# Optimization experiments

Hardware: AMD Instinct MI355X
Metric: run time of the kernel (lower is better)

## Reference

```python
import jax, jax.numpy as jnp
import numpy as np

B, S, D, H, E, K = 2, 2048, 512, 2048, 16, 2
LN_EPS = 1e-5


def setup_inputs() -> dict:
    key = jax.random.key(0)
    ks = jax.random.split(key, 9)
    s_in = 1.0 / np.sqrt(D)
    s_hid = 1.0 / np.sqrt(H)
    return {
        "x": jax.random.normal(ks[0], (B, S, D), dtype=jnp.float32),
        "Wg": jax.random.normal(ks[1], (D, E), dtype=jnp.float32) * s_in,
        "bg": jax.random.normal(ks[2], (E,), dtype=jnp.float32) * 0.01,
        "W1": jax.random.normal(ks[3], (E, D, H), dtype=jnp.float32) * s_in,
        "b1": jax.random.normal(ks[4], (E, H), dtype=jnp.float32) * 0.01,
        "W2": jax.random.normal(ks[5], (E, H, D), dtype=jnp.float32) * s_hid,
        "b2": jax.random.normal(ks[6], (E, D), dtype=jnp.float32) * 0.01,
        "gamma": jnp.ones((D,), dtype=jnp.float32),
        "beta": jnp.zeros((D,), dtype=jnp.float32),
    }


def reference(x, Wg, bg, W1, b1, W2, b2, gamma, beta):
    # --- top-k gating (GatingFuncTopK) ---
    logits = jnp.einsum("bsd,de->bse", x, Wg) + bg            # [B,S,E]
    probs = jax.nn.softmax(logits, axis=-1)
    topk_vals, topk_idx = jax.lax.top_k(probs, K)             # [B,S,K]
    # scatter top-k probs back into a sparse [B,S,E] routing matrix
    sparse = (jax.nn.one_hot(topk_idx, E, dtype=probs.dtype)
              * topk_vals[..., None]).sum(axis=-2)            # [B,S,E]

    # --- dense all-expert FFN (stack over experts, as in the torch code) ---
    h = jax.nn.relu(jnp.einsum("bsd,edh->ebsh", x, W1)
                    + b1[:, None, None, :])                   # [E,B,S,H]
    ex = jnp.einsum("ebsh,ehd->ebsd", h, W2) + b2[:, None, None, :]  # [E,B,S,D]

    # --- weighted combine + residual + layernorm ---
    out = jnp.einsum("bse,ebsd->bsd", sparse, ex) + x
    mu = out.mean(axis=-1, keepdims=True)
    var = ((out - mu) ** 2).mean(axis=-1, keepdims=True)
    out = (out - mu) * jax.lax.rsqrt(var + LN_EPS) * gamma + beta
    return out
```

## Files before the change

### kernel.cpp

```cpp
#include <hip/hip_runtime.h>
#include <math.h>

#define NTOK 4096
#define DDIM 512
#define HDIM 2048
#define NEXP 16


#define WS_COUNTS    0u
#define WS_OFFSETS   1024u
#define WS_NTILES    1280u
#define WS_TM        1536u
#define WS_EPOS      4096u
#define WS_TOK       36864u
#define WS_WL        299008u
#define WS_XA        1048576u
#define WS_W1T       11534336u
#define WS_W2T       45088768u
#define WS_HB        78643200u
#define WS_YB        WS_W1T

typedef __attribute__((ext_vector_type(8))) short short8;
typedef __attribute__((ext_vector_type(4))) float floatx4;
typedef unsigned short ushort_t;

__device__ __forceinline__ ushort_t f2bf(float f) {
    unsigned u = __float_as_uint(f);
    u += 0x7fffu + ((u >> 16) & 1u);
    return (ushort_t)(u >> 16);
}
__device__ __forceinline__ float bf2f(ushort_t u) {
    return __uint_as_float((unsigned)u << 16);
}

#define BAR_LGKM() asm volatile("s_waitcnt lgkmcnt(0)\n\ts_barrier" ::: "memory")

__global__ __launch_bounds__(256) void prep_kernel(
    const float* __restrict__ x, const float* __restrict__ Wg,
    const float* __restrict__ bg, const float* __restrict__ W1,
    const float* __restrict__ W2, int* __restrict__ counts,
    int* __restrict__ tok_list, float* __restrict__ w_list,
    int* __restrict__ epos, ushort_t* __restrict__ W1t,
    ushort_t* __restrict__ W2t)
{
    __shared__ __align__(16) float smem[4416];
    __shared__ int lcnt[16], lbase[16];
    const int tid = threadIdx.x;
    int bid = blockIdx.x;

    if (bid < 512) {
        float (*xs)[520] = (float(*)[520])smem;
        float (*lsm)[16][2] = (float(*)[16][2])(smem + 4160);
        const int t0 = bid * 8;
        const float* xg = x + (size_t)t0 * DDIM;
        #pragma unroll
        for (int p = 0; p < 4; ++p) {
            const int idx = p * 1024 + tid * 4;
            *(float4*)&xs[idx >> 9][idx & 511] = *(const float4*)(xg + idx);
        }
        if (tid < 16) lcnt[tid] = 0;
        __syncthreads();
        const int tl = tid >> 5, e = (tid >> 1) & 15, h = tid & 1;
        float a0 = 0.f, a1 = 0.f, a2 = 0.f, a3 = 0.f;
        #pragma unroll 8
        for (int it = 0; it < 64; ++it) {
            const int d = h * 256 + it * 4;
            const float4 xv = *(const float4*)&xs[tl][d];
            a0 = fmaf(xv.x, Wg[(d + 0) * 16 + e], a0);
            a1 = fmaf(xv.y, Wg[(d + 1) * 16 + e], a1);
            a2 = fmaf(xv.z, Wg[(d + 2) * 16 + e], a2);
            a3 = fmaf(xv.w, Wg[(d + 3) * 16 + e], a3);
        }
        lsm[tl][e][h] = (a0 + a1) + (a2 + a3);
        __syncthreads();

        int i0 = 0, i1 = -1, r0 = 0, r1 = 0;
        float w0 = 0.f, w1 = 0.f;
        const bool tokth = ((tid & 31) == 0);
        if (tokth) {
            float l[16];
            #pragma unroll
            for (int j = 0; j < NEXP; ++j) l[j] = lsm[tl][j][0] + lsm[tl][j][1] + bg[j];
            float m = -1e30f;
            #pragma unroll
            for (int j = 0; j < NEXP; ++j) m = fmaxf(m, l[j]);
            float s = 0.f;
            #pragma unroll
            for (int j = 0; j < NEXP; ++j) s += __expf(l[j] - m);
            float v0 = -1e30f;
            #pragma unroll
            for (int j = 0; j < NEXP; ++j)
                if (l[j] > v0) { v0 = l[j]; i0 = j; }
            float v1 = -1e30f;
            #pragma unroll
            for (int j = 0; j < NEXP; ++j)
                if (j != i0 && l[j] > v1) { v1 = l[j]; i1 = j; }
            w0 = __expf(v0 - m) / s;
            w1 = __expf(v1 - m) / s;
            r0 = atomicAdd(&lcnt[i0], 1);
            r1 = atomicAdd(&lcnt[i1], 1);
        }
        __syncthreads();
        if (tid < 16 && lcnt[tid] > 0)
            lbase[tid] = atomicAdd(&counts[tid * 16], lcnt[tid]);
        __syncthreads();
        if (tokth) {
            const int t = t0 + tl;
            const int p0 = lbase[i0] + r0;
            tok_list[i0 * NTOK + p0] = t;
            w_list[i0 * NTOK + p0] = w0;
            epos[t * 2 + 0] = (i0 << 16) | p0;
            const int p1 = lbase[i1] + r1;
            tok_list[i1 * NTOK + p1] = t;
            w_list[i1 * NTOK + p1] = w1;
            epos[t * 2 + 1] = (i1 << 16) | p1;
        }
        return;
    }

    bid -= 512;
    unsigned* lds32 = (unsigned*)smem;
    const float* src; ushort_t* dst; int C, NT, CK, e, n0, ktbase;
    if (bid < 1024) {
        e = bid >> 6; const int q = bid & 63;
        src = W1; dst = W1t; C = HDIM; NT = 128; CK = 64;
        n0 = (q & 31) << 6; ktbase = (q >> 5) << 2;
    } else {
        bid -= 1024;
        e = bid >> 6; const int q = bid & 63;
        src = W2; dst = W2t; C = DDIM; NT = 32; CK = 256;
        n0 = (q & 7) << 6; ktbase = (q >> 3) << 2;
    }
    const int kq = tid >> 4, cc4 = (tid & 15) << 2;
    const int w = tid >> 6, l = tid & 63;
    const float* sp = src + (size_t)e * (DDIM * HDIM) + n0;
    ushort_t* run = dst + ((size_t)e * NT + (n0 >> 4) + w) * ((size_t)CK * 128);

    float4 v[2][4];
    #pragma unroll
    for (int p = 0; p < 4; ++p)
        v[0][p] = *(const float4*)(sp + (size_t)((ktbase + 0) * 64 + kq * 4 + p) * C + cc4);
    #pragma unroll
    for (int p = 0; p < 4; ++p)
        v[1][p] = *(const float4*)(sp + (size_t)((ktbase + 1) * 64 + kq * 4 + p) * C + cc4);

    #pragma unroll
    for (int i = 0; i < 4; ++i) {
        unsigned* lb = lds32 + (i & 1) * 2112;
        const float4* vv = v[i & 1];
        #pragma unroll
        for (int p2 = 0; p2 < 2; ++p2) {
            const float4 a = vv[2 * p2], b = vv[2 * p2 + 1];
            const int kp = kq * 2 + p2;
            lb[(cc4 + 0) * 33 + kp] = (unsigned)f2bf(a.x) | ((unsigned)f2bf(b.x) << 16);
            lb[(cc4 + 1) * 33 + kp] = (unsigned)f2bf(a.y) | ((unsigned)f2bf(b.y) << 16);
            lb[(cc4 + 2) * 33 + kp] = (unsigned)f2bf(a.z) | ((unsigned)f2bf(b.z) << 16);
            lb[(cc4 + 3) * 33 + kp] = (unsigned)f2bf(a.w) | ((unsigned)f2bf(b.w) << 16);
        }
        if (i < 2) {
            #pragma unroll
            for (int p = 0; p < 4; ++p)
                v[i & 1][p] = *(const float4*)(
                    sp + (size_t)((ktbase + i + 2) * 64 + kq * 4 + p) * C + cc4);
        }
        BAR_LGKM();
        const int kt = ktbase + i;
        ushort_t* runp = run + (size_t)kt * 1024;
        #pragma unroll
        for (int s = 0; s < 2; ++s) {
            const int kc = s * 4 + (l >> 4);
            const unsigned* rp = lb + (w * 16 + (l & 15)) * 33 + kc * 4;
            const unsigned o0 = rp[0], o1 = rp[1], o2 = rp[2], o3 = rp[3];
            *(uint4*)(runp + (size_t)s * 512 + l * 8) = make_uint4(o0, o1, o2, o3);
        }
    }
}

__global__ void scan_kernel(const int* __restrict__ counts, int* __restrict__ offsets,
                            int* __restrict__ tm, int* __restrict__ ntiles)
{
    const int lane = threadIdx.x;
    int c = (lane < NEXP) ? counts[lane * 16] : 0;
    int t = (c + 127) >> 7;
    int ic = c, it = t;
    #pragma unroll
    for (int off = 1; off < 16; off <<= 1) {
        const int pc = __shfl_up(ic, off, 64);
        const int pt = __shfl_up(it, off, 64);
        if (lane >= off) { ic += pc; it += pt; }
    }
    if (lane < NEXP) {
        offsets[lane] = ic - c;
        if (lane == NEXP - 1) { offsets[NEXP] = ic; ntiles[0] = it; }
        const int tb = it - t;
        for (int i = 0; i < t; ++i) tm[tb + i] = (lane << 16) | i;
    }
}

__global__ __launch_bounds__(256) void gather_xa(
    const float* __restrict__ x, const int* __restrict__ tok_list,
    const int* __restrict__ counts, const int* __restrict__ tm,
    const int* __restrict__ ntiles, ushort_t* __restrict__ xa)
{
    const int b = blockIdx.x;
    if (b >= ntiles[0]) return;
    const int info = tm[b];
    const int e = info >> 16, m0 = (info & 0xffff) << 7;
    const int Me = counts[e * 16];
    const int row = threadIdx.x >> 1;
    const int half = threadIdx.x & 1;
    const int kbase = blockIdx.y * 128 + half * 64;
    const int tok = tok_list[e * NTOK + min(m0 + row, Me - 1)];
    const float* src = x + (size_t)tok * DDIM + kbase;
    ushort_t* dstb = xa + (size_t)b * 65536 + (size_t)(row >> 4) * 8192 + (row & 15) * 8;
    #pragma unroll
    for (int q = 0; q < 16; ++q) {
        const int k = kbase + q * 4;
        const float4 v = *(const float4*)(src + q * 4);
        ushort4 o = make_ushort4(f2bf(v.x), f2bf(v.y), f2bf(v.z), f2bf(v.w));
        *(ushort4*)(dstb + (size_t)(k >> 3) * 128 + (k & 7)) = o;
    }
}

__global__ __launch_bounds__(256) void gemm1_mfma(
    const ushort_t* __restrict__ xa, const ushort_t* __restrict__ W1t,
    const float* __restrict__ b1, const int* __restrict__ tm,
    const int* __restrict__ ntiles, ushort_t* __restrict__ hb)
{
    const int t = blockIdx.y;
    if (t >= ntiles[0]) return;
    const int e = tm[t] >> 16;
    const int n0 = blockIdx.x << 7;
    const int tid = threadIdx.x, lane = tid & 63, w = tid >> 6;
    const int fm = lane & 15, fq = lane >> 4;
    const int wr = (w >> 1) << 6, wc = (w & 1) << 6;

    const ushort_t* baseA = xa + (size_t)t * 65536
                          + (size_t)((w >> 1) * 4) * 8192 + lane * 8;
    const ushort_t* baseB = W1t + ((size_t)e * 128 + (n0 >> 4) + (w & 1) * 4) * 8192
                          + lane * 8;

    floatx4 acc[4][4] = {};
    #pragma unroll 4
    for (int kc = 0; kc < 16; ++kc) {
        short8 af[4], bf[4];
        #pragma unroll
        for (int i = 0; i < 4; ++i)
            af[i] = *(const short8*)(baseA + i * 8192 + kc * 512);
        #pragma unroll
        for (int j = 0; j < 4; ++j)
            bf[j] = *(const short8*)(baseB + j * 8192 + kc * 512);
        #pragma unroll
        for (int i = 0; i < 4; ++i)
            #pragma unroll
            for (int j = 0; j < 4; ++j)
                acc[i][j] = __builtin_amdgcn_mfma_f32_16x16x32_bf16(
                    af[i], bf[j], acc[i][j], 0, 0, 0);
    }

    __shared__ ushort_t ls[128 * 128];
    #pragma unroll
    for (int j = 0; j < 4; ++j) {
        const float bias = b1[(size_t)e * HDIM + n0 + wc + j * 16 + fm];
        #pragma unroll
        for (int i = 0; i < 4; ++i)
            #pragma unroll
            for (int r = 0; r < 4; ++r) {
                const int row = wr + i * 16 + fq * 4 + r;
                ls[row * 128 + wc + j * 16 + fm] =
                    f2bf(fmaxf(acc[i][j][r] + bias, 0.f));
            }
    }
    __syncthreads();
    ushort_t* hbase = hb + (size_t)t * 262144 + (size_t)(n0 >> 3) * 128;
    #pragma unroll
    for (int p = 0; p < 8; ++p) {
        const int unit = tid + p * 256;
        const int row = unit >> 4, c16 = unit & 15;
        *(short8*)(hbase + (size_t)(row >> 4) * 32768 + (size_t)c16 * 128
                   + (row & 15) * 8) = *(const short8*)&ls[row * 128 + c16 * 8];
    }
}

__global__ __launch_bounds__(256) void gemm2_mfma(
    const ushort_t* __restrict__ hb, const ushort_t* __restrict__ W2t,
    const float* __restrict__ b2, const float* __restrict__ w_list,
    const int* __restrict__ counts, const int* __restrict__ offsets,
    const int* __restrict__ tm, const int* __restrict__ ntiles,
    ushort_t* __restrict__ yb)
{
    const int t = blockIdx.y;
    if (t >= ntiles[0]) return;
    const int info = tm[t];
    const int e = info >> 16, m0 = (info & 0xffff) << 7;
    const int Me = counts[e * 16], aoff = offsets[e];
    const int n0 = blockIdx.x << 7;
    const int kz = blockIdx.z;
    const int tid = threadIdx.x, lane = tid & 63, w = tid >> 6;
    const int fm = lane & 15, fq = lane >> 4;
    const int wr = (w >> 1) << 6, wc = (w & 1) << 6;

    const ushort_t* baseA = hb + (size_t)t * 262144
                          + (size_t)((w >> 1) * 4) * 32768 + kz * 16384 + lane * 8;
    const ushort_t* baseB = W2t + ((size_t)e * 32 + (n0 >> 4) + (w & 1) * 4) * 32768
                          + kz * 16384 + lane * 8;

    floatx4 acc[4][4] = {};
    #pragma unroll 4
    for (int kc = 0; kc < 32; ++kc) {
        short8 af[4], bf[4];
        #pragma unroll
        for (int i = 0; i < 4; ++i)
            af[i] = *(const short8*)(baseA + i * 32768 + kc * 512);
        #pragma unroll
        for (int j = 0; j < 4; ++j)
            bf[j] = *(const short8*)(baseB + j * 32768 + kc * 512);
        #pragma unroll
        for (int i = 0; i < 4; ++i)
            #pragma unroll
            for (int j = 0; j < 4; ++j)
                acc[i][j] = __builtin_amdgcn_mfma_f32_16x16x32_bf16(
                    af[i], bf[j], acc[i][j], 0, 0, 0);
    }

    __shared__ ushort_t ls[128 * 128];
    #pragma unroll
    for (int j = 0; j < 4; ++j) {
        const float bias = (kz == 0) ? b2[(size_t)e * DDIM + n0 + wc + j * 16 + fm] : 0.f;
        #pragma unroll
        for (int i = 0; i < 4; ++i)
            #pragma unroll
            for (int r = 0; r < 4; ++r) {
                const int row = wr + i * 16 + fq * 4 + r;
                const float gw = w_list[e * NTOK + min(m0 + row, Me - 1)];
                ls[row * 128 + wc + j * 16 + fm] = f2bf(gw * (acc[i][j][r] + bias));
            }
    }
    __syncthreads();
    ushort_t* ybase = yb + (size_t)kz * (8192 * 512) + n0;
    #pragma unroll
    for (int p = 0; p < 8; ++p) {
        const int unit = tid + p * 256;
        const int row = unit >> 4, c16 = unit & 15;
        if (m0 + row < Me)
            *(short8*)(ybase + (size_t)(aoff + m0 + row) * 512 + c16 * 8)
                = *(const short8*)&ls[row * 128 + c16 * 8];
    }
}

__global__ __launch_bounds__(256) void ln_kernel(
    const float* __restrict__ x, const ushort_t* __restrict__ yb,
    const int* __restrict__ epos, const int* __restrict__ offsets,
    const float* __restrict__ gamma, const float* __restrict__ beta,
    float* __restrict__ out)
{
    const int t = blockIdx.x * 4 + (threadIdx.x >> 6);
    const int lane = threadIdx.x & 63;
    const int d0 = lane * 8;

    const int p0 = epos[2 * t + 0];
    const int p1 = epos[2 * t + 1];
    const size_t r0 = (size_t)(offsets[p0 >> 16] + (p0 & 0xFFFF));
    const size_t r1 = (size_t)(offsets[p1 >> 16] + (p1 & 0xFFFF));

    const short8 y0 = *(const short8*)(yb + r0 * 512 + d0);
    const short8 y1 = *(const short8*)(yb + (size_t)8192 * 512 + r0 * 512 + d0);
    const short8 y2 = *(const short8*)(yb + r1 * 512 + d0);
    const short8 y3 = *(const short8*)(yb + (size_t)8192 * 512 + r1 * 512 + d0);
    float xv[8];
    *(float4*)&xv[0] = *(const float4*)(x + (size_t)t * DDIM + d0);
    *(float4*)&xv[4] = *(const float4*)(x + (size_t)t * DDIM + d0 + 4);

    float v[8];
    float s = 0.f;
    #pragma unroll
    for (int i = 0; i < 8; ++i) {
        v[i] = xv[i] + bf2f((ushort_t)y0[i]) + bf2f((ushort_t)y1[i])
                     + bf2f((ushort_t)y2[i]) + bf2f((ushort_t)y3[i]);
        s += v[i];
    }
    #pragma unroll
    for (int o = 32; o > 0; o >>= 1) s += __shfl_xor(s, o, 64);
    const float mu = s * (1.f / DDIM);
    float q = 0.f;
    #pragma unroll
    for (int i = 0; i < 8; ++i) { const float d_ = v[i] - mu; q = fmaf(d_, d_, q); }
    #pragma unroll
    for (int o = 32; o > 0; o >>= 1) q += __shfl_xor(q, o, 64);
    const float rstd = rsqrtf(q * (1.f / DDIM) + 1e-5f);

    float g[8], bt[8], o8[8];
    *(float4*)&g[0] = *(const float4*)(gamma + d0);
    *(float4*)&g[4] = *(const float4*)(gamma + d0 + 4);
    *(float4*)&bt[0] = *(const float4*)(beta + d0);
    *(float4*)&bt[4] = *(const float4*)(beta + d0 + 4);
    #pragma unroll
    for (int i = 0; i < 8; ++i) o8[i] = (v[i] - mu) * rstd * g[i] + bt[i];
    *(float4*)(out + (size_t)t * DDIM + d0) = *(float4*)&o8[0];
    *(float4*)(out + (size_t)t * DDIM + d0 + 4) = *(float4*)&o8[4];
}

extern "C" void kernel_launch(void* const* d_in, const int* in_sizes, int n_in,
                              void* d_out, int out_size, void* d_ws, size_t ws_size,
                              hipStream_t stream) {
    const float* x     = (const float*)d_in[0];
    const float* Wg    = (const float*)d_in[1];
    const float* bg    = (const float*)d_in[2];
    const float* W1    = (const float*)d_in[3];
    const float* b1    = (const float*)d_in[4];
    const float* W2    = (const float*)d_in[5];
    const float* b2    = (const float*)d_in[6];
    const float* gamma = (const float*)d_in[7];
    const float* beta  = (const float*)d_in[8];
    float* out = (float*)d_out;

    char* ws = (char*)d_ws;
    int*      counts   = (int*)(ws + WS_COUNTS);
    int*      offsets  = (int*)(ws + WS_OFFSETS);
    int*      ntiles   = (int*)(ws + WS_NTILES);
    int*      tm       = (int*)(ws + WS_TM);
    int*      epos     = (int*)(ws + WS_EPOS);
    int*      tok_list = (int*)(ws + WS_TOK);
    float*    w_list   = (float*)(ws + WS_WL);
    ushort_t* xa       = (ushort_t*)(ws + WS_XA);
    ushort_t* W1t      = (ushort_t*)(ws + WS_W1T);
    ushort_t* W2t      = (ushort_t*)(ws + WS_W2T);
    ushort_t* hb       = (ushort_t*)(ws + WS_HB);
    ushort_t* yb       = (ushort_t*)(ws + WS_YB);

    hipMemsetAsync(counts, 0, 1024, stream);
    prep_kernel<<<2560, 256, 0, stream>>>(x, Wg, bg, W1, W2, counts,
                                          tok_list, w_list, epos, W1t, W2t);
    scan_kernel<<<1, 64, 0, stream>>>(counts, offsets, tm, ntiles);
    gather_xa<<<dim3(80, 4), 256, 0, stream>>>(x, tok_list, counts, tm, ntiles, xa);
    gemm1_mfma<<<dim3(HDIM / 128, 80), 256, 0, stream>>>(
        xa, W1t, b1, tm, ntiles, hb);
    gemm2_mfma<<<dim3(DDIM / 128, 80, 2), 256, 0, stream>>>(
        hb, W2t, b2, w_list, counts, offsets, tm, ntiles, yb);
    ln_kernel<<<NTOK / 4, 256, 0, stream>>>(x, yb, epos, offsets, gamma, beta, out);
}
```

Measured before the change: 301.0 us.

## Stage expert GEMM tiles through double-buffered LDS and deepen gemm2 split-K

Both expert GEMMs now copy A and B tiles into a double-buffered shared-memory stage using global_load_lds, prefetching the next K chunk while MFMAs run on the current one. Before, each wave read its operands straight from global memory, and waves sharing a tile loaded the same data twice. gemm2's split-K grows from 2 to 4 slices to put more blocks on the GPU, so the LayerNorm kernel now sums 8 bf16 partials per token. The prep kernel is also split into separate gating and weight-transpose launches. The costs are a barrier every K iteration, more partial-output traffic, and one extra kernel launch.

Measured after the change: 299.9 us. Within noise of the previous version (-0.4%).

```diff
diff --git a/kernel.cpp b/kernel.cpp
--- a/kernel.cpp
+++ b/kernel.cpp
@@ -33,93 +33,101 @@
     return __uint_as_float((unsigned)u << 16);
 }
 
+__device__ __forceinline__ void gld16(const void* g, void* l) {
+    __builtin_amdgcn_global_load_lds(
+        (const __attribute__((address_space(1))) unsigned*)g,
+        (__attribute__((address_space(3))) unsigned*)l, 16, 0, 0);
+}
+
 #define BAR_LGKM() asm volatile("s_waitcnt lgkmcnt(0)\n\ts_barrier" ::: "memory")
 
-__global__ __launch_bounds__(256) void prep_kernel(
+__global__ __launch_bounds__(256) void gating_kernel(
     const float* __restrict__ x, const float* __restrict__ Wg,
-    const float* __restrict__ bg, const float* __restrict__ W1,
-    const float* __restrict__ W2, int* __restrict__ counts,
+    const float* __restrict__ bg, int* __restrict__ counts,
     int* __restrict__ tok_list, float* __restrict__ w_list,
-    int* __restrict__ epos, ushort_t* __restrict__ W1t,
-    ushort_t* __restrict__ W2t)
+    int* __restrict__ epos)
 {
     __shared__ __align__(16) float smem[4416];
     __shared__ int lcnt[16], lbase[16];
     const int tid = threadIdx.x;
+    const int bid = blockIdx.x;
+
+    float (*xs)[520] = (float(*)[520])smem;
+    float (*lsm)[16][2] = (float(*)[16][2])(smem + 4160);
+    const int t0 = bid * 8;
+    const float* xg = x + (size_t)t0 * DDIM;
+    #pragma unroll
+    for (int p = 0; p < 4; ++p) {
+        const int idx = p * 1024 + tid * 4;
+        *(float4*)&xs[idx >> 9][idx & 511] = *(const float4*)(xg + idx);
+    }
+    if (tid < 16) lcnt[tid] = 0;
+    __syncthreads();
+    const int tl = tid >> 5, e = (tid >> 1) & 15, h = tid & 1;
+    float a0 = 0.f, a1 = 0.f, a2 = 0.f, a3 = 0.f;
+    #pragma unroll 8
+    for (int it = 0; it < 64; ++it) {
+        const int d = h * 256 + it * 4;
+        const float4 xv = *(const float4*)&xs[tl][d];
+        a0 = fmaf(xv.x, Wg[(d + 0) * 16 + e], a0);
+        a1 = fmaf(xv.y, Wg[(d + 1) * 16 + e], a1);
+        a2 = fmaf(xv.z, Wg[(d + 2) * 16 + e], a2);
+        a3 = fmaf(xv.w, Wg[(d + 3) * 16 + e], a3);
+    }
+    lsm[tl][e][h] = (a0 + a1) + (a2 + a3);
+    __syncthreads();
+
+    int i0 = 0, i1 = -1, r0 = 0, r1 = 0;
+    float w0 = 0.f, w1 = 0.f;
+    const bool tokth = ((tid & 31) == 0);
+    if (tokth) {
+        float l[16];
+        #pragma unroll
+        for (int j = 0; j < NEXP; ++j) l[j] = lsm[tl][j][0] + lsm[tl][j][1] + bg[j];
+        float m = -1e30f;
+        #pragma unroll
+        for (int j = 0; j < NEXP; ++j) m = fmaxf(m, l[j]);
+        float s = 0.f;
+        #pragma unroll
+        for (int j = 0; j < NEXP; ++j) s += __expf(l[j] - m);
+        float v0 = -1e30f;
+        #pragma unroll
+        for (int j = 0; j < NEXP; ++j)
+            if (l[j] > v0) { v0 = l[j]; i0 = j; }
+        float v1 = -1e30f;
+        #pragma unroll
+        for (int j = 0; j < NEXP; ++j)
+            if (j != i0 && l[j] > v1) { v1 = l[j]; i1 = j; }
+        w0 = __expf(v0 - m) / s;
+        w1 = __expf(v1 - m) / s;
+        r0 = atomicAdd(&lcnt[i0], 1);
+        r1 = atomicAdd(&lcnt[i1], 1);
+    }
+    __syncthreads();
+    if (tid < 16 && lcnt[tid] > 0)
+        lbase[tid] = atomicAdd(&counts[tid * 16], lcnt[tid]);
+    __syncthreads();
+    if (tokth) {
+        const int t = t0 + tl;
+        const int p0 = lbase[i0] + r0;
+        tok_list[i0 * NTOK + p0] = t;
+        w_list[i0 * NTOK + p0] = w0;
+        epos[t * 2 + 0] = (i0 << 16) | p0;
+        const int p1 = lbase[i1] + r1;
+        tok_list[i1 * NTOK + p1] = t;
+        w_list[i1 * NTOK + p1] = w1;
+        epos[t * 2 + 1] = (i1 << 16) | p1;
+    }
+}
+
+__global__ __launch_bounds__(256) void wtrans_kernel(
+    const float* __restrict__ W1, const float* __restrict__ W2,
+    ushort_t* __restrict__ W1t, ushort_t* __restrict__ W2t)
+{
+    __shared__ __align__(16) unsigned lds32[4224];
+    const int tid = threadIdx.x;
     int bid = blockIdx.x;
 
-    if (bid < 512) {
-        float (*xs)[520] = (float(*)[520])smem;
-        float (*lsm)[16][2] = (float(*)[16][2])(smem + 4160);
-        const int t0 = bid * 8;
-        const float* xg = x + (size_t)t0 * DDIM;
-        #pragma unroll
-        for (int p = 0; p < 4; ++p) {
-            const int idx = p * 1024 + tid * 4;
-            *(float4*)&xs[idx >> 9][idx & 511] = *(const float4*)(xg + idx);
-        }
-        if (tid < 16) lcnt[tid] = 0;
-        __syncthreads();
-        const int tl = tid >> 5, e = (tid >> 1) & 15, h = tid & 1;
-        float a0 = 0.f, a1 = 0.f, a2 = 0.f, a3 = 0.f;
-        #pragma unroll 8
-        for (int it = 0; it < 64; ++it) {
-            const int d = h * 256 + it * 4;
-            const float4 xv = *(const float4*)&xs[tl][d];
-            a0 = fmaf(xv.x, Wg[(d + 0) * 16 + e], a0);
-            a1 = fmaf(xv.y, Wg[(d + 1) * 16 + e], a1);
-            a2 = fmaf(xv.z, Wg[(d + 2) * 16 + e], a2);
-            a3 = fmaf(xv.w, Wg[(d + 3) * 16 + e], a3);
-        }
-        lsm[tl][e][h] = (a0 + a1) + (a2 + a3);
-        __syncthreads();
-
-        int i0 = 0, i1 = -1, r0 = 0, r1 = 0;
-        float w0 = 0.f, w1 = 0.f;
-        const bool tokth = ((tid & 31) == 0);
-        if (tokth) {
-            float l[16];
-            #pragma unroll
-            for (int j = 0; j < NEXP; ++j) l[j] = lsm[tl][j][0] + lsm[tl][j][1] + bg[j];
-            float m = -1e30f;
-            #pragma unroll
-            for (int j = 0; j < NEXP; ++j) m = fmaxf(m, l[j]);
-            float s = 0.f;
-            #pragma unroll
-            for (int j = 0; j < NEXP; ++j) s += __expf(l[j] - m);
-            float v0 = -1e30f;
-            #pragma unroll
-            for (int j = 0; j < NEXP; ++j)
-                if (l[j] > v0) { v0 = l[j]; i0 = j; }
-            float v1 = -1e30f;
-            #pragma unroll
-            for (int j = 0; j < NEXP; ++j)
-                if (j != i0 && l[j] > v1) { v1 = l[j]; i1 = j; }
-            w0 = __expf(v0 - m) / s;
-            w1 = __expf(v1 - m) / s;
-            r0 = atomicAdd(&lcnt[i0], 1);
-            r1 = atomicAdd(&lcnt[i1], 1);
-        }
-        __syncthreads();
-        if (tid < 16 && lcnt[tid] > 0)
-            lbase[tid] = atomicAdd(&counts[tid * 16], lcnt[tid]);
-        __syncthreads();
-        if (tokth) {
-            const int t = t0 + tl;
-            const int p0 = lbase[i0] + r0;
-            tok_list[i0 * NTOK + p0] = t;
-            w_list[i0 * NTOK + p0] = w0;
-            epos[t * 2 + 0] = (i0 << 16) | p0;
-            const int p1 = lbase[i1] + r1;
-            tok_list[i1 * NTOK + p1] = t;
-            w_list[i1 * NTOK + p1] = w1;
-            epos[t * 2 + 1] = (i1 << 16) | p1;
-        }
-        return;
-    }
-
-    bid -= 512;
-    unsigned* lds32 = (unsigned*)smem;
     const float* src; ushort_t* dst; int C, NT, CK, e, n0, ktbase;
     if (bid < 1024) {
         e = bid >> 6; const int q = bid & 63;
@@ -235,30 +243,45 @@
     const int fm = lane & 15, fq = lane >> 4;
     const int wr = (w >> 1) << 6, wc = (w & 1) << 6;
 
-    const ushort_t* baseA = xa + (size_t)t * 65536
-                          + (size_t)((w >> 1) * 4) * 8192 + lane * 8;
-    const ushort_t* baseB = W1t + ((size_t)e * 128 + (n0 >> 4) + (w & 1) * 4) * 8192
-                          + lane * 8;
+    __shared__ __align__(16) ushort_t lds[16384];
+
+    const ushort_t* gA = xa + (size_t)t * 65536 + lane * 8;
+    const ushort_t* gB = W1t + ((size_t)e * 128 + (n0 >> 4)) * 8192 + lane * 8;
+    const int s0 = w, s1 = w + 4;
+
+    #define G1_STAGE(d, kc) do {                                            \
+        ushort_t* lb_ = &lds[(d) * 8192];                                   \
+        gld16(gA + (size_t)s0 * 8192 + (kc) * 512, lb_ + s0 * 512);         \
+        gld16(gA + (size_t)s1 * 8192 + (kc) * 512, lb_ + s1 * 512);         \
+        gld16(gB + (size_t)s0 * 8192 + (kc) * 512, lb_ + 4096 + s0 * 512);  \
+        gld16(gB + (size_t)s1 * 8192 + (kc) * 512, lb_ + 4096 + s1 * 512);  \
+    } while (0)
+
+    G1_STAGE(0, 0);
+    __syncthreads();
 
     floatx4 acc[4][4] = {};
-    #pragma unroll 4
     for (int kc = 0; kc < 16; ++kc) {
+        const int d = kc & 1;
+        if (kc < 15) G1_STAGE(d ^ 1, kc + 1);
+        const ushort_t* la = &lds[d * 8192 + (wr >> 4) * 512 + lane * 8];
+        const ushort_t* lbB = &lds[d * 8192 + 4096 + (wc >> 4) * 512 + lane * 8];
         short8 af[4], bf[4];
         #pragma unroll
-        for (int i = 0; i < 4; ++i)
-            af[i] = *(const short8*)(baseA + i * 8192 + kc * 512);
-        #pragma unroll
-        for (int j = 0; j < 4; ++j)
-            bf[j] = *(const short8*)(baseB + j * 8192 + kc * 512);
+        for (int i = 0; i < 4; ++i) af[i] = *(const short8*)(la + i * 512);
+        #pragma unroll
+        for (int j = 0; j < 4; ++j) bf[j] = *(const short8*)(lbB + j * 512);
         #pragma unroll
         for (int i = 0; i < 4; ++i)
             #pragma unroll
             for (int j = 0; j < 4; ++j)
                 acc[i][j] = __builtin_amdgcn_mfma_f32_16x16x32_bf16(
                     af[i], bf[j], acc[i][j], 0, 0, 0);
-    }
-
-    __shared__ ushort_t ls[128 * 128];
+        __syncthreads();
+    }
+    #undef G1_STAGE
+
+    ushort_t* ls = lds;
     #pragma unroll
     for (int j = 0; j < 4; ++j) {
         const float bias = b1[(size_t)e * HDIM + n0 + wc + j * 16 + fm];
@@ -300,30 +323,46 @@
     const int fm = lane & 15, fq = lane >> 4;
     const int wr = (w >> 1) << 6, wc = (w & 1) << 6;
 
-    const ushort_t* baseA = hb + (size_t)t * 262144
-                          + (size_t)((w >> 1) * 4) * 32768 + kz * 16384 + lane * 8;
-    const ushort_t* baseB = W2t + ((size_t)e * 32 + (n0 >> 4) + (w & 1) * 4) * 32768
-                          + kz * 16384 + lane * 8;
+    __shared__ __align__(16) ushort_t lds[16384];
+
+    const ushort_t* gA = hb + (size_t)t * 262144 + (size_t)kz * 8192 + lane * 8;
+    const ushort_t* gB = W2t + ((size_t)e * 32 + (n0 >> 4)) * 32768
+                       + (size_t)kz * 8192 + lane * 8;
+    const int s0 = w, s1 = w + 4;
+
+    #define G2_STAGE(d, kc) do {                                            \
+        ushort_t* lb_ = &lds[(d) * 8192];                                   \
+        gld16(gA + (size_t)s0 * 32768 + (kc) * 512, lb_ + s0 * 512);        \
+        gld16(gA + (size_t)s1 * 32768 + (kc) * 512, lb_ + s1 * 512);        \
+        gld16(gB + (size_t)s0 * 32768 + (kc) * 512, lb_ + 4096 + s0 * 512); \
+        gld16(gB + (size_t)s1 * 32768 + (kc) * 512, lb_ + 4096 + s1 * 512); \
+    } while (0)
+
+    G2_STAGE(0, 0);
+    __syncthreads();
 
     floatx4 acc[4][4] = {};
-    #pragma unroll 4
-    for (int kc = 0; kc < 32; ++kc) {
+    for (int kc = 0; kc < 16; ++kc) {
+        const int d = kc & 1;
+        if (kc < 15) G2_STAGE(d ^ 1, kc + 1);
+        const ushort_t* la = &lds[d * 8192 + (wr >> 4) * 512 + lane * 8];
+        const ushort_t* lbB = &lds[d * 8192 + 4096 + (wc >> 4) * 512 + lane * 8];
         short8 af[4], bf[4];
         #pragma unroll
-        for (int i = 0; i < 4; ++i)
-            af[i] = *(const short8*)(baseA + i * 32768 + kc * 512);
-        #pragma unroll
-        for (int j = 0; j < 4; ++j)
-            bf[j] = *(const short8*)(baseB + j * 32768 + kc * 512);
+        for (int i = 0; i < 4; ++i) af[i] = *(const short8*)(la + i * 512);
+        #pragma unroll
+        for (int j = 0; j < 4; ++j) bf[j] = *(const short8*)(lbB + j * 512);
         #pragma unroll
         for (int i = 0; i < 4; ++i)
             #pragma unroll
             for (int j = 0; j < 4; ++j)
                 acc[i][j] = __builtin_amdgcn_mfma_f32_16x16x32_bf16(
                     af[i], bf[j], acc[i][j], 0, 0, 0);
-    }
-
-    __shared__ ushort_t ls[128 * 128];
+        __syncthreads();
+    }
+    #undef G2_STAGE
+
+    ushort_t* ls = lds;
     #pragma unroll
     for (int j = 0; j < 4; ++j) {
         const float bias = (kz == 0) ? b2[(size_t)e * DDIM + n0 + wc + j * 16 + fm] : 0.f;
@@ -363,10 +402,12 @@
     const size_t r0 = (size_t)(offsets[p0 >> 16] + (p0 & 0xFFFF));
     const size_t r1 = (size_t)(offsets[p1 >> 16] + (p1 & 0xFFFF));
 
-    const short8 y0 = *(const short8*)(yb + r0 * 512 + d0);
-    const short8 y1 = *(const short8*)(yb + (size_t)8192 * 512 + r0 * 512 + d0);
-    const short8 y2 = *(const short8*)(yb + r1 * 512 + d0);
-    const short8 y3 = *(const short8*)(yb + (size_t)8192 * 512 + r1 * 512 + d0);
+    short8 ys[8];
+    #pragma unroll
+    for (int kz = 0; kz < 4; ++kz) {
+        ys[kz * 2 + 0] = *(const short8*)(yb + (size_t)kz * (8192 * 512) + r0 * 512 + d0);
+        ys[kz * 2 + 1] = *(const short8*)(yb + (size_t)kz * (8192 * 512) + r1 * 512 + d0);
+    }
     float xv[8];
     *(float4*)&xv[0] = *(const float4*)(x + (size_t)t * DDIM + d0);
     *(float4*)&xv[4] = *(const float4*)(x + (size_t)t * DDIM + d0 + 4);
@@ -375,9 +416,11 @@
     float s = 0.f;
     #pragma unroll
     for (int i = 0; i < 8; ++i) {
-        v[i] = xv[i] + bf2f((ushort_t)y0[i]) + bf2f((ushort_t)y1[i])
-                     + bf2f((ushort_t)y2[i]) + bf2f((ushort_t)y3[i]);
-        s += v[i];
+        float a = xv[i];
+        #pragma unroll
+        for (int q = 0; q < 8; ++q) a += bf2f((ushort_t)ys[q][i]);
+        v[i] = a;
+        s += a;
     }
     #pragma unroll
     for (int o = 32; o > 0; o >>= 1) s += __shfl_xor(s, o, 64);
@@ -429,13 +472,13 @@
     ushort_t* yb       = (ushort_t*)(ws + WS_YB);
 
     hipMemsetAsync(counts, 0, 1024, stream);
-    prep_kernel<<<2560, 256, 0, stream>>>(x, Wg, bg, W1, W2, counts,
-                                          tok_list, w_list, epos, W1t, W2t);
+    gating_kernel<<<512, 256, 0, stream>>>(x, Wg, bg, counts, tok_list, w_list, epos);
+    wtrans_kernel<<<2048, 256, 0, stream>>>(W1, W2, W1t, W2t);
     scan_kernel<<<1, 64, 0, stream>>>(counts, offsets, tm, ntiles);
     gather_xa<<<dim3(80, 4), 256, 0, stream>>>(x, tok_list, counts, tm, ntiles, xa);
     gemm1_mfma<<<dim3(HDIM / 128, 80), 256, 0, stream>>>(
         xa, W1t, b1, tm, ntiles, hb);
-    gemm2_mfma<<<dim3(DDIM / 128, 80, 2), 256, 0, stream>>>(
+    gemm2_mfma<<<dim3(DDIM / 128, 80, 4), 256, 0, stream>>>(
         hb, W2t, b2, w_list, counts, offsets, tm, ntiles, yb);
     ln_kernel<<<NTOK / 4, 256, 0, stream>>>(x, yb, epos, offsets, gamma, beta, out);
 }
```
